# Optimization experiments

Measured on AMD Instinct MI355X. Metric: run time of the kernel, lower is better.

## Reference

```python
import jax, jax.numpy as jnp
import numpy as np
from jax import lax

EPS = 1e-5
DN = ('NCHW', 'OIHW', 'NCHW')


def ternarize(w):
    # Standard TWN-style ternarization: {-1, 0, +1} with threshold 0.7*mean|w|
    thr = 0.7 * jnp.mean(jnp.abs(w))
    return jnp.sign(w) * (jnp.abs(w) > thr).astype(w.dtype)


def conv(x, w, b=None):
    y = lax.conv_general_dilated(x, w, (1, 1), 'VALID', dimension_numbers=DN)
    if b is not None:
        y = y + b[None, :, None, None]
    return y


def bn(x, g, be, m, v):
    inv = g / jnp.sqrt(v + EPS)
    return x * inv[None, :, None, None] + (be - m * inv)[None, :, None, None]


def maxpool2(x):
    return lax.reduce_window(x, -jnp.inf, lax.max, (1, 1, 2, 2), (1, 1, 2, 2), 'VALID')


def setup_inputs() -> dict:
    key = jax.random.key(0)
    ks = jax.random.split(key, 21)
    d = {}
    d['x'] = jax.random.normal(ks[0], (8192, 1, 28, 28), jnp.float32)
    d['w1'] = ternarize(jax.random.normal(ks[1], (32, 1, 5, 5), jnp.float32))
    d['b1'] = jax.random.normal(ks[2], (32,), jnp.float32) * 0.1
    d['g1'] = jax.random.uniform(ks[3], (32,), jnp.float32, 0.5, 1.5)
    d['be1'] = jax.random.normal(ks[4], (32,), jnp.float32) * 0.1
    d['m1'] = jax.random.normal(ks[5], (32,), jnp.float32) * 0.1
    d['v1'] = jax.random.uniform(ks[6], (32,), jnp.float32, 0.5, 1.5)
    d['w2'] = ternarize(jax.random.normal(ks[7], (64, 32, 5, 5), jnp.float32))
    d['b2'] = jax.random.normal(ks[8], (64,), jnp.float32) * 0.1
    d['g2'] = jax.random.uniform(ks[9], (64,), jnp.float32, 0.5, 1.5)
    d['be2'] = jax.random.normal(ks[10], (64,), jnp.float32) * 0.1
    d['m2'] = jax.random.normal(ks[11], (64,), jnp.float32) * 0.1
    d['v2'] = jax.random.uniform(ks[12], (64,), jnp.float32, 0.5, 1.5)
    d['w3'] = ternarize(jax.random.normal(ks[13], (512, 1024, 1, 1), jnp.float32))
    d['b3'] = jax.random.normal(ks[14], (512,), jnp.float32) * 0.1
    d['g3'] = jax.random.uniform(ks[15], (512,), jnp.float32, 0.5, 1.5)
    d['be3'] = jax.random.normal(ks[16], (512,), jnp.float32) * 0.1
    d['m3'] = jax.random.normal(ks[17], (512,), jnp.float32) * 0.1
    d['v3'] = jax.random.uniform(ks[18], (512,), jnp.float32, 0.5, 1.5)
    d['w4'] = jax.random.normal(ks[19], (10, 512, 1, 1), jnp.float32) * 0.05
    return d


def reference(x, w1, b1, g1, be1, m1, v1, w2, b2, g2, be2, m2, v2,
              w3, b3, g3, be3, m3, v3, w4):
    h = conv(x, w1, b1)                       # [B,32,24,24]
    h = maxpool2(jax.nn.relu(bn(h, g1, be1, m1, v1)))   # [B,32,12,12]
    h = conv(h, w2, b2)                       # [B,64,8,8]
    h = maxpool2(jax.nn.relu(bn(h, g2, be2, m2, v2)))   # [B,64,4,4]
    h = h.reshape(-1, 1024, 1, 1)             # flatten C,H,W
    h = jax.nn.relu(bn(conv(h, w3, b3), g3, be3, m3, v3))  # [B,512,1,1]
    h = conv(h, w4)                            # [B,10,1,1]
    return h.reshape(-1, 10)
```

## Files before the change

kernel.cpp:

```cpp
#include <hip/hip_runtime.h>

#define EPS 1e-5f

typedef float f32x4 __attribute__((ext_vector_type(4)));
typedef short short8_t __attribute__((ext_vector_type(8)));
typedef unsigned int uint4v __attribute__((ext_vector_type(4)));
typedef unsigned short ushort_t;

__global__ void prep_kernel(const float* __restrict__ b1, const float* __restrict__ g1,
                            const float* __restrict__ be1, const float* __restrict__ m1,
                            const float* __restrict__ v1,
                            const float* __restrict__ b2, const float* __restrict__ g2,
                            const float* __restrict__ be2, const float* __restrict__ m2,
                            const float* __restrict__ v2,
                            const float* __restrict__ b3, const float* __restrict__ g3,
                            const float* __restrict__ be3, const float* __restrict__ m3,
                            const float* __restrict__ v3,
                            const float* __restrict__ w1, const float* __restrict__ w2,
                            const float* __restrict__ w3,
                            ushort_t* __restrict__ w1frag, ushort_t* __restrict__ w2frag,
                            ushort_t* __restrict__ w3frag, float* __restrict__ prm) {
  int tid = blockIdx.x * blockDim.x + threadIdx.x;
  int stride = gridDim.x * blockDim.x;
  for (int c = tid; c < 32; c += stride) {
    float s = g1[c] / sqrtf(v1[c] + EPS);
    prm[c] = s;
    prm[32 + c] = (b1[c] - m1[c]) * s + be1[c];
  }
  for (int c = tid; c < 64; c += stride) {
    float s = g2[c] / sqrtf(v2[c] + EPS);
    prm[64 + c] = s;
    prm[128 + c] = (b2[c] - m2[c]) * s + be2[c];
  }
  for (int c = tid; c < 512; c += stride) {
    float s = g3[c] / sqrtf(v3[c] + EPS);
    prm[192 + c] = s;
    prm[704 + c] = (b3[c] - m3[c]) * s + be3[c];
  }
  for (int i = tid; i < 2 * 2 * 64 * 8; i += stride) {
    const int j = i & 7;
    const int l = (i >> 3) & 63;
    const int nt = (i >> 9) & 1;
    const int p = i >> 10;
    const int oc = nt * 16 + (l & 15);
    const int t = (l >> 4) * 8 + j;
    const float v = (t < 25) ? w1[oc * 25 + t] : 0.f;
    const unsigned u = __float_as_uint(v);
    const ushort_t hi = (ushort_t)(u >> 16);
    const float r = v - __uint_as_float(u & 0xffff0000u);
    const ushort_t lo = (ushort_t)(__float_as_uint(r) >> 16);
    w1frag[i] = p ? lo : hi;
  }
  for (int i = tid; i < 25 * 4 * 64 * 8; i += stride) {
    const int kk = i >> 11;
    const int r = i & 2047;
    const int nt = r >> 9;
    const int r2 = r & 511;
    const int l = r2 >> 3;
    const int j = r2 & 7;
    const int oc = nt * 16 + (l & 15);
    const int ic = (l >> 4) * 8 + j;
    w2frag[i] = (ushort_t)(__float_as_uint(w2[oc * 800 + ic * 25 + kk]) >> 16);
  }
  for (int i = tid; i < 32 * 32 * 64 * 8; i += stride) {
    const int ks = i >> 14;
    const int r = i & 16383;
    const int ntg = r >> 9;
    const int r2 = r & 511;
    const int l = r2 >> 3;
    const int j = r2 & 7;
    const int oc = ntg * 16 + (l & 15);
    const int k = ks * 32 + (l >> 4) * 8 + j;
    w3frag[i] = (ushort_t)(__float_as_uint(w3[oc * 1024 + k]) >> 16);
  }
}

__launch_bounds__(128)
__global__ void conv12_kernel(const float* __restrict__ x,
                              const ushort_t* __restrict__ w1frag,
                              const ushort_t* __restrict__ w2frag,
                              const float* __restrict__ prm,
                              ushort_t* __restrict__ h2pH, ushort_t* __restrict__ h2pL) {
  __shared__ __align__(16) unsigned char lds[26240];

  const int tid = threadIdx.x;
  const int w = tid >> 6, l = tid & 63;
  const int b = blockIdx.x;
  const int m15 = l & 15, g = l >> 4;

  unsigned* imgP = (unsigned*)lds;
  ushort_t* insA = (ushort_t*)(lds + 3200);

  const float* xb = x + (size_t)b * 784;
  for (int i = tid; i < 784; i += 128) {
    const float v = xb[i];
    const unsigned u = __float_as_uint(v);
    const float r = v - __uint_as_float(u & 0xffff0000u);
    imgP[i] = (u & 0xffff0000u) | (__float_as_uint(r) >> 16);
  }
  if (tid < 16) imgP[784 + tid] = 0u;

  short8_t B1h[2], B1l[2];
#pragma unroll
  for (int nt = 0; nt < 2; ++nt) {
    B1h[nt] = *(const short8_t*)(w1frag + (size_t)(nt * 64 + l) * 8);
    B1l[nt] = *(const short8_t*)(w1frag + (size_t)((2 + nt) * 64 + l) * 8);
  }

  int off[8];
#pragma unroll
  for (int j = 0; j < 8; ++j) {
    const int t = g * 8 + j;
    const int ky = t / 5, kx = t - ky * 5;
    off[j] = (t < 25) ? (ky * 28 + kx) : 0;
  }

  float s1[2], sh1[2], s2[4], sh2[4];
#pragma unroll
  for (int nt = 0; nt < 2; ++nt) {
    s1[nt] = prm[nt * 16 + m15];
    sh1[nt] = prm[32 + nt * 16 + m15];
  }
#pragma unroll
  for (int nt = 0; nt < 4; ++nt) {
    s2[nt] = prm[64 + nt * 16 + m15];
    sh2[nt] = prm[128 + nt * 16 + m15];
  }
  __syncthreads();

#pragma unroll 1
  for (int i = 0; i < 18; ++i) {
    const int mt = w * 18 + i;
    const int q = mt * 16 + m15;
    const int p_pool = q >> 2, sub = q & 3;
    const int py = p_pool / 12, px = p_pool - py * 12;
    const int Y = 2 * py + (sub >> 1), X = 2 * px + (sub & 1);
    const unsigned* pixb = imgP + Y * 28 + X;
    unsigned pv[8];
#pragma unroll
    for (int j = 0; j < 8; ++j) pv[j] = pixb[off[j]];
    uint4v hv, lv;
#pragma unroll
    for (int k = 0; k < 4; ++k) {
      hv[k] = (pv[2 * k] >> 16) | (pv[2 * k + 1] & 0xffff0000u);
      lv[k] = (pv[2 * k] & 0xffffu) | (pv[2 * k + 1] << 16);
    }
    const short8_t ah = __builtin_bit_cast(short8_t, hv);
    const short8_t al = __builtin_bit_cast(short8_t, lv);

    f32x4 c0 = {0.f, 0.f, 0.f, 0.f}, c1 = {0.f, 0.f, 0.f, 0.f};
    c0 = __builtin_amdgcn_mfma_f32_16x16x32_bf16(ah, B1h[0], c0, 0, 0, 0);
    c1 = __builtin_amdgcn_mfma_f32_16x16x32_bf16(ah, B1h[1], c1, 0, 0, 0);
    c0 = __builtin_amdgcn_mfma_f32_16x16x32_bf16(al, B1h[0], c0, 0, 0, 0);
    c1 = __builtin_amdgcn_mfma_f32_16x16x32_bf16(al, B1h[1], c1, 0, 0, 0);
    c0 = __builtin_amdgcn_mfma_f32_16x16x32_bf16(ah, B1l[0], c0, 0, 0, 0);
    c1 = __builtin_amdgcn_mfma_f32_16x16x32_bf16(ah, B1l[1], c1, 0, 0, 0);

    const int cell = mt * 4 + g;
#pragma unroll
    for (int nt = 0; nt < 2; ++nt) {
      const f32x4 c = nt ? c1 : c0;
      const float pvv = fmaxf(fmaxf(c[0], c[1]), fmaxf(c[2], c[3]));
      const float a = fmaxf(fmaf(pvv, s1[nt], sh1[nt]), 0.f);
      const unsigned u = __float_as_uint(a);
      const float r = a - __uint_as_float(u & 0xffff0000u);
      const int ic = nt * 16 + m15;
      insA[cell * 40 + ic] = (ushort_t)(u >> 16);
      insA[5760 + cell * 40 + ic] = (ushort_t)(__float_as_uint(r) >> 16);
    }
  }
  __syncthreads();

  const int sy = (m15 & 3) >> 1, sx = m15 & 1;
  const int X2 = 2 * (m15 >> 2) + sx;

  f32x4 acc[2][4];
#pragma unroll
  for (int m = 0; m < 2; ++m)
#pragma unroll
    for (int nt = 0; nt < 4; ++nt) acc[m][nt] = (f32x4){0.f, 0.f, 0.f, 0.f};

#pragma unroll 1
  for (int pass = 0; pass < 5; ++pass) {
    short8_t wr[5][4];
#pragma unroll
    for (int kx = 0; kx < 5; ++kx)
#pragma unroll
      for (int nt = 0; nt < 4; ++nt)
        wr[kx][nt] = *(const short8_t*)(w2frag + (size_t)(((pass * 5 + kx) * 4 + nt) * 64 + l) * 8);
#pragma unroll
    for (int kx = 0; kx < 5; ++kx) {
#pragma unroll
      for (int m = 0; m < 2; ++m) {
        const int mt2 = 2 * w + m;
        const int cellin = (2 * mt2 + sy + pass) * 12 + X2 + kx;
        const short8_t aH = *(const short8_t*)(insA + cellin * 40 + g * 8);
        const short8_t aL = *(const short8_t*)(insA + 5760 + cellin * 40 + g * 8);
#pragma unroll
        for (int nt = 0; nt < 4; ++nt) {
          acc[m][nt] = __builtin_amdgcn_mfma_f32_16x16x32_bf16(aH, wr[kx][nt], acc[m][nt], 0, 0, 0);
          acc[m][nt] = __builtin_amdgcn_mfma_f32_16x16x32_bf16(aL, wr[kx][nt], acc[m][nt], 0, 0, 0);
        }
      }
    }
  }

  const size_t ob = (size_t)b * 1024;
#pragma unroll
  for (int m = 0; m < 2; ++m) {
    const int cell2 = (2 * w + m) * 4 + g;
#pragma unroll
    for (int nt = 0; nt < 4; ++nt) {
      const f32x4 c = acc[m][nt];
      const float pvv = fmaxf(fmaxf(c[0], c[1]), fmaxf(c[2], c[3]));
      const float a = fmaxf(fmaf(pvv, s2[nt], sh2[nt]), 0.f);
      const unsigned u = __float_as_uint(a);
      const float r = a - __uint_as_float(u & 0xffff0000u);
      const int oc = nt * 16 + m15;
      h2pH[ob + oc * 16 + cell2] = (ushort_t)(u >> 16);
      h2pL[ob + oc * 16 + cell2] = (ushort_t)(__float_as_uint(r) >> 16);
    }
  }
}

__launch_bounds__(256)
__global__ void fc3_kernel(const ushort_t* __restrict__ h2pH, const ushort_t* __restrict__ h2pL,
                           const ushort_t* __restrict__ w3frag, const float* __restrict__ prm,
                           float* __restrict__ a3) {
  const int orig = blockIdx.x + (blockIdx.y << 2);
  const int xcd = orig & 7;
  const int j = orig >> 3;
  const int ytile = (xcd << 4) | (j >> 2);
  const int xtile = j & 3;
  const int n0 = xtile * 128;
  const int m0 = ytile * 64;
  const int w = threadIdx.x >> 6, l = threadIdx.x & 63;
  const int mrow = m0 + w * 16 + (l & 15);
  const int kc8 = (l >> 4) * 8;

  const ushort_t* aHp = h2pH + (size_t)mrow * 1024 + kc8;
  const ushort_t* aLp = h2pL + (size_t)mrow * 1024 + kc8;
  const ushort_t* bp = w3frag + (size_t)(n0 >> 4) * 512 + (size_t)l * 8;

  f32x4 acc[8];
#pragma unroll
  for (int t = 0; t < 8; ++t) acc[t] = (f32x4){0.f, 0.f, 0.f, 0.f};

#pragma unroll 2
  for (int ks = 0; ks < 32; ++ks) {
    const short8_t aH = *(const short8_t*)(aHp + ks * 32);
    const short8_t aL = *(const short8_t*)(aLp + ks * 32);
    const ushort_t* bks = bp + (size_t)ks * 16384;
#pragma unroll
    for (int t = 0; t < 8; ++t) {
      const short8_t bb = *(const short8_t*)(bks + t * 512);
      acc[t] = __builtin_amdgcn_mfma_f32_16x16x32_bf16(aH, bb, acc[t], 0, 0, 0);
      acc[t] = __builtin_amdgcn_mfma_f32_16x16x32_bf16(aL, bb, acc[t], 0, 0, 0);
    }
  }

#pragma unroll
  for (int t = 0; t < 8; ++t) {
    const int oc = n0 + t * 16 + (l & 15);
    const float s = prm[192 + oc], sh = prm[704 + oc];
#pragma unroll
    for (int r = 0; r < 4; ++r) {
      const int m = m0 + w * 16 + (l >> 4) * 4 + r;
      a3[(size_t)m * 512 + oc] = fmaxf(fmaf(acc[t][r], s, sh), 0.f);
    }
  }
}

__launch_bounds__(256)
__global__ void fc4_kernel(const float* __restrict__ a3, const float* __restrict__ w4,
                           float* __restrict__ out, int B) {
  const int w = threadIdx.x >> 6, l = threadIdx.x & 63;
  const int b = blockIdx.x * 4 + w;
  if (b >= B) return;
  const float4* ar = (const float4*)(a3 + (size_t)b * 512);
  const float4 a0 = ar[l * 2];
  const float4 a1 = ar[l * 2 + 1];
#pragma unroll
  for (int j = 0; j < 10; ++j) {
    const float4* wr = (const float4*)(w4 + j * 512);
    const float4 w0 = wr[l * 2];
    const float4 w1 = wr[l * 2 + 1];
    float sv = a0.x * w0.x + a0.y * w0.y + a0.z * w0.z + a0.w * w0.w +
               a1.x * w1.x + a1.y * w1.y + a1.z * w1.z + a1.w * w1.w;
#pragma unroll
    for (int off = 1; off < 64; off <<= 1) sv += __shfl_xor(sv, off);
    if (l == 0) out[(size_t)b * 10 + j] = sv;
  }
}

extern "C" void kernel_launch(void* const* d_in, const int* in_sizes, int n_in,
                              void* d_out, int out_size, void* d_ws, size_t ws_size,
                              hipStream_t stream) {
  const float* x  = (const float*)d_in[0];
  const float* w1 = (const float*)d_in[1];
  const float* b1 = (const float*)d_in[2];
  const float* g1 = (const float*)d_in[3];
  const float* be1 = (const float*)d_in[4];
  const float* m1 = (const float*)d_in[5];
  const float* v1 = (const float*)d_in[6];
  const float* w2 = (const float*)d_in[7];
  const float* b2 = (const float*)d_in[8];
  const float* g2 = (const float*)d_in[9];
  const float* be2 = (const float*)d_in[10];
  const float* m2 = (const float*)d_in[11];
  const float* v2 = (const float*)d_in[12];
  const float* w3 = (const float*)d_in[13];
  const float* b3 = (const float*)d_in[14];
  const float* g3 = (const float*)d_in[15];
  const float* be3 = (const float*)d_in[16];
  const float* m3 = (const float*)d_in[17];
  const float* v3 = (const float*)d_in[18];
  const float* w4 = (const float*)d_in[19];

  const int B = in_sizes[0] / 784;

  float* prm = (float*)d_ws;
  ushort_t* w1frag = (ushort_t*)(prm + 1216);
  ushort_t* w2frag = w1frag + 2048;
  ushort_t* w3frag = w2frag + 51200;
  ushort_t* h2pH = w3frag + 524288;
  ushort_t* h2pL = h2pH + (size_t)B * 1024;
  float* a3 = (float*)(h2pL + (size_t)B * 1024);

  prep_kernel<<<256, 256, 0, stream>>>(b1, g1, be1, m1, v1, b2, g2, be2, m2, v2,
                                       b3, g3, be3, m3, v3, w1, w2, w3,
                                       w1frag, w2frag, w3frag, prm);
  conv12_kernel<<<B, 128, 0, stream>>>(x, w1frag, w2frag, prm, h2pH, h2pL);
  dim3 g3d(4, B / 64);
  fc3_kernel<<<g3d, 256, 0, stream>>>(h2pH, h2pL, w3frag, prm, a3);
  fc4_kernel<<<(B + 3) / 4, 256, 0, stream>>>(a3, w4, (float*)d_out, B);
}
```

Baseline: 262.7 us.

## Double-buffer conv2 weight loads and retile fc3 into 64x64 XCD-mapped tiles

In conv12, the per-pass load of all five kx weight fragments is replaced by two half-buffers (3 and 2 kx) loaded one step ahead of the MFMA work, so global weight fetches overlap compute. The first weight loads are placed before the LDS barrier, and launch bounds now request 3 waves per EU. fc3 moves from 64x128 to 64x64 output tiles with a 1D grid of 1024 blocks, remaps blocks so an XCD shares M tiles, and unrolls the K loop deeper. The trade-off is more register pressure from the prefetch buffers and twice as many activation reads in fc3. The fc3 grid is now hardcoded for B=8192.

```diff
diff --git a/kernel.cpp b/kernel.cpp
--- a/kernel.cpp
+++ b/kernel.cpp
@@ -75,7 +75,34 @@
   }
 }
 
-__launch_bounds__(128)
+#define LOADW(BUF, P, H) { \
+  const int kxb_ = (H) ? 3 : 0; \
+  const int nkx_ = (H) ? 2 : 3; \
+  _Pragma("unroll") \
+  for (int kx_ = 0; kx_ < 3; ++kx_) if (kx_ < nkx_) { \
+    _Pragma("unroll") \
+    for (int nt_ = 0; nt_ < 4; ++nt_) \
+      BUF[kx_][nt_] = *(const short8_t*)(w2frag + \
+          (size_t)((((P) * 5 + kxb_ + kx_) * 4 + nt_) * 64 + l) * 8); \
+  } }
+
+#define COMPW(BUF, P, H) { \
+  const int kxb_ = (H) ? 3 : 0; \
+  const int nkx_ = (H) ? 2 : 3; \
+  _Pragma("unroll") \
+  for (int kx_ = 0; kx_ < 3; ++kx_) if (kx_ < nkx_) { \
+    _Pragma("unroll") \
+    for (int m_ = 0; m_ < 2; ++m_) { \
+      const int cellin_ = (2 * (2 * w + m_) + sy + (P)) * 12 + X2 + kxb_ + kx_; \
+      const short8_t aH_ = *(const short8_t*)(insA + cellin_ * 40 + g * 8); \
+      const short8_t aL_ = *(const short8_t*)(insA + 5760 + cellin_ * 40 + g * 8); \
+      _Pragma("unroll") \
+      for (int nt_ = 0; nt_ < 4; ++nt_) { \
+        acc[m_][nt_] = __builtin_amdgcn_mfma_f32_16x16x32_bf16(aH_, BUF[kx_][nt_], acc[m_][nt_], 0, 0, 0); \
+        acc[m_][nt_] = __builtin_amdgcn_mfma_f32_16x16x32_bf16(aL_, BUF[kx_][nt_], acc[m_][nt_], 0, 0, 0); \
+      } } } }
+
+__launch_bounds__(128, 3)
 __global__ void conv12_kernel(const float* __restrict__ x,
                               const ushort_t* __restrict__ w1frag,
                               const ushort_t* __restrict__ w2frag,
@@ -169,7 +196,6 @@
       insA[5760 + cell * 40 + ic] = (ushort_t)(__float_as_uint(r) >> 16);
     }
   }
-  __syncthreads();
 
   const int sy = (m15 & 3) >> 1, sx = m15 & 1;
   const int X2 = 2 * (m15 >> 2) + sx;
@@ -180,30 +206,21 @@
 #pragma unroll
     for (int nt = 0; nt < 4; ++nt) acc[m][nt] = (f32x4){0.f, 0.f, 0.f, 0.f};
 
-#pragma unroll 1
-  for (int pass = 0; pass < 5; ++pass) {
-    short8_t wr[5][4];
-#pragma unroll
-    for (int kx = 0; kx < 5; ++kx)
-#pragma unroll
-      for (int nt = 0; nt < 4; ++nt)
-        wr[kx][nt] = *(const short8_t*)(w2frag + (size_t)(((pass * 5 + kx) * 4 + nt) * 64 + l) * 8);
-#pragma unroll
-    for (int kx = 0; kx < 5; ++kx) {
-#pragma unroll
-      for (int m = 0; m < 2; ++m) {
-        const int mt2 = 2 * w + m;
-        const int cellin = (2 * mt2 + sy + pass) * 12 + X2 + kx;
-        const short8_t aH = *(const short8_t*)(insA + cellin * 40 + g * 8);
-        const short8_t aL = *(const short8_t*)(insA + 5760 + cellin * 40 + g * 8);
-#pragma unroll
-        for (int nt = 0; nt < 4; ++nt) {
-          acc[m][nt] = __builtin_amdgcn_mfma_f32_16x16x32_bf16(aH, wr[kx][nt], acc[m][nt], 0, 0, 0);
-          acc[m][nt] = __builtin_amdgcn_mfma_f32_16x16x32_bf16(aL, wr[kx][nt], acc[m][nt], 0, 0, 0);
-        }
-      }
-    }
-  }
+  short8_t wrA[3][4], wrB[3][4];
+  LOADW(wrA, 0, 0)
+  LOADW(wrB, 0, 1)
+  __syncthreads();
+
+  COMPW(wrA, 0, 0) LOADW(wrA, 1, 0)
+  COMPW(wrB, 0, 1) LOADW(wrB, 1, 1)
+  COMPW(wrA, 1, 0) LOADW(wrA, 2, 0)
+  COMPW(wrB, 1, 1) LOADW(wrB, 2, 1)
+  COMPW(wrA, 2, 0) LOADW(wrA, 3, 0)
+  COMPW(wrB, 2, 1) LOADW(wrB, 3, 1)
+  COMPW(wrA, 3, 0) LOADW(wrA, 4, 0)
+  COMPW(wrB, 3, 1) LOADW(wrB, 4, 1)
+  COMPW(wrA, 4, 0)
+  COMPW(wrB, 4, 1)
 
   const size_t ob = (size_t)b * 1024;
 #pragma unroll
@@ -227,13 +244,13 @@
 __global__ void fc3_kernel(const ushort_t* __restrict__ h2pH, const ushort_t* __restrict__ h2pL,
                            const ushort_t* __restrict__ w3frag, const float* __restrict__ prm,
                            float* __restrict__ a3) {
-  const int orig = blockIdx.x + (blockIdx.y << 2);
-  const int xcd = orig & 7;
-  const int j = orig >> 3;
-  const int ytile = (xcd << 4) | (j >> 2);
-  const int xtile = j & 3;
-  const int n0 = xtile * 128;
-  const int m0 = ytile * 64;
+  const int id = blockIdx.x;
+  const int xcd = id & 7;
+  const int r = id >> 3;
+  const int xt = r & 7;
+  const int yt = ((r >> 3) << 3) | xcd;
+  const int n0 = xt * 64;
+  const int m0 = yt * 64;
   const int w = threadIdx.x >> 6, l = threadIdx.x & 63;
   const int mrow = m0 + w * 16 + (l & 15);
   const int kc8 = (l >> 4) * 8;
@@ -242,17 +259,17 @@
   const ushort_t* aLp = h2pL + (size_t)mrow * 1024 + kc8;
   const ushort_t* bp = w3frag + (size_t)(n0 >> 4) * 512 + (size_t)l * 8;
 
-  f32x4 acc[8];
-#pragma unroll
-  for (int t = 0; t < 8; ++t) acc[t] = (f32x4){0.f, 0.f, 0.f, 0.f};
-
-#pragma unroll 2
+  f32x4 acc[4];
+#pragma unroll
+  for (int t = 0; t < 4; ++t) acc[t] = (f32x4){0.f, 0.f, 0.f, 0.f};
+
+#pragma unroll 4
   for (int ks = 0; ks < 32; ++ks) {
     const short8_t aH = *(const short8_t*)(aHp + ks * 32);
     const short8_t aL = *(const short8_t*)(aLp + ks * 32);
     const ushort_t* bks = bp + (size_t)ks * 16384;
 #pragma unroll
-    for (int t = 0; t < 8; ++t) {
+    for (int t = 0; t < 4; ++t) {
       const short8_t bb = *(const short8_t*)(bks + t * 512);
       acc[t] = __builtin_amdgcn_mfma_f32_16x16x32_bf16(aH, bb, acc[t], 0, 0, 0);
       acc[t] = __builtin_amdgcn_mfma_f32_16x16x32_bf16(aL, bb, acc[t], 0, 0, 0);
@@ -260,13 +277,13 @@
   }
 
 #pragma unroll
-  for (int t = 0; t < 8; ++t) {
+  for (int t = 0; t < 4; ++t) {
     const int oc = n0 + t * 16 + (l & 15);
     const float s = prm[192 + oc], sh = prm[704 + oc];
 #pragma unroll
-    for (int r = 0; r < 4; ++r) {
-      const int m = m0 + w * 16 + (l >> 4) * 4 + r;
-      a3[(size_t)m * 512 + oc] = fmaxf(fmaf(acc[t][r], s, sh), 0.f);
+    for (int rr = 0; rr < 4; ++rr) {
+      const int m = m0 + w * 16 + (l >> 4) * 4 + rr;
+      a3[(size_t)m * 512 + oc] = fmaxf(fmaf(acc[t][rr], s, sh), 0.f);
     }
   }
 }
@@ -331,7 +348,6 @@
                                        b3, g3, be3, m3, v3, w1, w2, w3,
                                        w1frag, w2frag, w3frag, prm);
   conv12_kernel<<<B, 128, 0, stream>>>(x, w1frag, w2frag, prm, h2pH, h2pL);
-  dim3 g3d(4, B / 64);
-  fc3_kernel<<<g3d, 256, 0, stream>>>(h2pH, h2pL, w3frag, prm, a3);
+  fc3_kernel<<<1024, 256, 0, stream>>>(h2pH, h2pL, w3frag, prm, a3);
   fc4_kernel<<<(B + 3) / 4, 256, 0, stream>>>(a3, w4, (float*)d_out, B);
 }
```

Measured after the change: 269.9 us. 2.7% more time.
